# Optimization experiments

Measured on AMD Instinct MI355X. Metric: run time of the kernel, lower is better.

The kernel has to match this reference:

```python
import jax, jax.numpy as jnp
import numpy as np

B, S, E, H = 2, 2048, 1024, 16
D = E // H  # head dim = 64


def setup_inputs() -> dict:
    key = jax.random.key(0)
    k1, k2, k3 = jax.random.split(key, 3)
    x = jax.random.normal(k1, (B, S, E), dtype=jnp.float32)
    W_attn = jax.random.normal(k2, (E, 3 * E), dtype=jnp.float32) * (1.0 / np.sqrt(E))
    b_attn = jnp.zeros((3 * E,), dtype=jnp.float32)
    W_proj = jax.random.normal(k3, (E, E), dtype=jnp.float32) * (1.0 / np.sqrt(E))
    b_proj = jnp.zeros((E,), dtype=jnp.float32)
    return {"x": x, "W_attn": W_attn, "b_attn": b_attn, "W_proj": W_proj, "b_proj": b_proj}


def reference(x, W_attn, b_attn, W_proj, b_proj):
    b, s, e = x.shape
    qkv = x @ W_attn + b_attn                      # (B, S, 3E)
    q, k, v = jnp.split(qkv, 3, axis=-1)
    # (B, S, E) -> (B, H, S, D)
    def heads(t):
        return t.reshape(b, s, H, D).transpose(0, 2, 1, 3)
    q, k, v = heads(q), heads(k), heads(v)
    scale = 1.0 / np.sqrt(D)
    # ring QK^T over world_size=1 == full QK^T; scores (B, H, S, S)
    attn = jnp.einsum("bhqd,bhkd->bhqk", q, k) * scale
    causal = jnp.tril(jnp.ones((s, s), dtype=bool))
    attn = jnp.where(causal[None, None], attn, -jnp.inf)
    attn = jax.nn.softmax(attn, axis=-1)
    # ring AV over world_size=1 == full AV
    y = jnp.einsum("bhqk,bhkd->bhqd", attn, v)     # (B, H, S, D)
    y = y.transpose(0, 2, 1, 3).reshape(b, s, e)   # (B, S, E)
    return y @ W_proj + b_proj
```

## Files before the change

### kernel.cpp

```cpp
#include <hip/hip_runtime.h>
#include <hip/hip_bf16.h>

#define B_ 2
#define S_ 2048
#define E_ 1024
#define H_ 16
#define D_ 64

typedef __attribute__((ext_vector_type(8))) _Float16 half8;
typedef __attribute__((ext_vector_type(4))) _Float16 half4;
typedef __attribute__((ext_vector_type(4))) float floatx4;

__device__ inline void gload16(const _Float16* g, _Float16* l) {
    __builtin_amdgcn_global_load_lds(
        (const __attribute__((address_space(1))) void*)g,
        (__attribute__((address_space(3))) void*)l, 16, 0, 0);
}

__global__ __launch_bounds__(256) void k_prep(const float* __restrict__ x, _Float16* __restrict__ xh,
                                              const float* __restrict__ Wa, _Float16* __restrict__ Wat,
                                              const float* __restrict__ Wp, _Float16* __restrict__ Wpt) {
    __shared__ _Float16 tile[32][33];
    int bid = blockIdx.x, tid = threadIdx.x;
    if (bid < 2048) {
        int i = (bid * 256 + tid) * 8;
        float4 a = *(const float4*)(x + i);
        float4 b = *(const float4*)(x + i + 4);
        half8 o;
        o[0] = (_Float16)a.x; o[1] = (_Float16)a.y; o[2] = (_Float16)a.z; o[3] = (_Float16)a.w;
        o[4] = (_Float16)b.x; o[5] = (_Float16)b.y; o[6] = (_Float16)b.z; o[7] = (_Float16)b.w;
        *(half8*)(xh + i) = o;
        return;
    }
    const float* in;
    _Float16* out;
    int R, C, bx, by;
    if (bid < 5120) {
        int t = bid - 2048;
        in = Wa; out = Wat; R = E_; C = 3 * E_;
        bx = t % 96; by = t / 96;
    } else {
        int t = bid - 5120;
        in = Wp; out = Wpt; R = E_; C = E_;
        bx = t & 31; by = t >> 5;
    }
    int tx = tid & 31, ty = tid >> 5;
    int c0 = bx * 32, r0 = by * 32;
#pragma unroll
    for (int k = 0; k < 4; k++) {
        int r = ty + k * 8;
        tile[r][tx] = (_Float16)in[(size_t)(r0 + r) * C + c0 + tx];
    }
    __syncthreads();
#pragma unroll
    for (int k = 0; k < 4; k++) {
        int r = ty + k * 8;
        out[(size_t)(c0 + r) * R + r0 + tx] = tile[tx][r];
    }
}

template <int MODE>
__global__ __launch_bounds__(256) void k_gemm(const _Float16* __restrict__ A,
                                              const _Float16* __restrict__ Bt,
                                              const float* __restrict__ bias,
                                              void* __restrict__ out0,
                                              _Float16* __restrict__ out1,
                                              _Float16* __restrict__ out2,
                                              int M, int N, int K) {
    __shared__ __align__(16) _Float16 As[128 * 32];
    __shared__ __align__(16) _Float16 Bs[128 * 32];
    int tid = threadIdx.x;
    int lane = tid & 63, w = tid >> 6;
    int wm = w >> 1, wn = w & 1;
    int l15 = lane & 15, quad = lane >> 4;
    int m0 = blockIdx.y * 128, n0 = blockIdx.x * 128;

    floatx4 acc[4][4];
    floatx4 zero = {0.f, 0.f, 0.f, 0.f};
#pragma unroll
    for (int i = 0; i < 4; i++)
#pragma unroll
        for (int j = 0; j < 4; j++) acc[i][j] = zero;

    for (int k0 = 0; k0 < K; k0 += 32) {
        __syncthreads();
#pragma unroll
        for (int c = 0; c < 2; c++) {
            int flat = c * 2048 + tid * 8;
            int row = flat >> 5, col = flat & 31;
            gload16(A + (size_t)(m0 + row) * K + k0 + col, &As[c * 2048 + w * 512]);
            gload16(Bt + (size_t)(n0 + row) * K + k0 + col, &Bs[c * 2048 + w * 512]);
        }
        __syncthreads();
        half8 af[4], bfr[4];
#pragma unroll
        for (int i = 0; i < 4; i++) af[i] = *(const half8*)&As[(wm * 64 + i * 16 + l15) * 32 + quad * 8];
#pragma unroll
        for (int j = 0; j < 4; j++) bfr[j] = *(const half8*)&Bs[(wn * 64 + j * 16 + l15) * 32 + quad * 8];
#pragma unroll
        for (int i = 0; i < 4; i++)
#pragma unroll
            for (int j = 0; j < 4; j++)
                acc[i][j] = __builtin_amdgcn_mfma_f32_16x16x32_f16(af[i], bfr[j], acc[i][j], 0, 0, 0);
    }
#pragma unroll
    for (int j = 0; j < 4; j++) {
        int gcol = n0 + wn * 64 + j * 16 + l15;
        float bj = bias[gcol];
        int sect = gcol >> 10, e = gcol & 1023;
        int hh = e >> 6, dd = e & 63;
#pragma unroll
        for (int i = 0; i < 4; i++) {
            int grow = m0 + wm * 64 + i * 16 + quad * 4;
#pragma unroll
            for (int r = 0; r < 4; r++) {
                float v = acc[i][j][r] + bj;
                if (MODE == 1) {
                    ((float*)out0)[(size_t)(grow + r) * N + gcol] = v;
                } else {
                    int row = grow + r;
                    int bb = row >> 11, ss = row & 2047;
                    size_t hb = (size_t)(bb * H_ + hh);
                    _Float16 v16 = (_Float16)v;
                    if (sect == 0)
                        ((_Float16*)out0)[(hb * S_ + ss) * D_ + dd] = v16;
                    else if (sect == 1)
                        out1[(hb * S_ + ss) * D_ + dd] = v16;
                    else
                        out2[(hb * D_ + dd) * S_ + ss] = v16;
                }
            }
        }
    }
}

__global__ __launch_bounds__(512, 4)
void k_attn(const _Float16* __restrict__ Qh,
            const _Float16* __restrict__ Kh,
            const _Float16* __restrict__ Vt,
            _Float16* __restrict__ y) {
    __shared__ __align__(16) _Float16 smem_h[25600];
    int tid = threadIdx.x;
    int lane = tid & 63, w = tid >> 6;
    int l15 = lane & 15, quad = lane >> 4;
    _Float16* KsB = smem_h;
    _Float16* VsB = smem_h + 8192;
    _Float16* Pw = smem_h + 16384 + w * (16 * 72);

    int bidx = blockIdx.x;
    int bh = 4 * (bidx & 7) + ((bidx >> 3) & 3);
    int qidx = (bidx >> 5) & 7;
    int qb = (bidx >> 8) ? qidx : (15 - qidx);
    int b = bh >> 4, h = bh & 15;

    const size_t hbase = (size_t)bh * (S_ * D_);
    const _Float16* Qp = Qh + hbase;
    const _Float16* Kp = Kh + hbase;
    const _Float16* Vp = Vt + hbase;

    int q0w = qb * 128 + 16 * w;
    int ktd = q0w >> 6;
    int ktmax = 2 * qb + 1;

    int r0 = tid >> 3;
    int cbh = ((tid * 8) & 63) ^ ((r0 & 7) << 3);
    const _Float16* kS = Kp + (size_t)r0 * D_ + cbh;
    const _Float16* vS = Vp + (size_t)r0 * S_ + cbh;

#define STAGE(kt_, buf_)                                             \
    do {                                                             \
        gload16(kS + (size_t)(kt_) * 4096, KsB + (buf_) * 4096 + w * 512); \
        gload16(vS + (size_t)(kt_) * 64, VsB + (buf_) * 4096 + w * 512);   \
    } while (0)

    half8 aq[2];
#pragma unroll
    for (int kk = 0; kk < 2; kk++) {
        half8 q = *(const half8*)(Qp + (size_t)(q0w + l15) * D_ + kk * 32 + quad * 8);
#pragma unroll
        for (int u = 0; u < 8; u++) q[u] *= (_Float16)0.125f;
        aq[kk] = q;
    }

    floatx4 zero = {0.f, 0.f, 0.f, 0.f};
    floatx4 o[4];
#pragma unroll
    for (int f = 0; f < 4; f++) o[f] = zero;
    float l_run = 0.f;

    STAGE(0, 0);
    int cur = 0;
    int swz = (l15 & 7) << 3;
    for (int kt = 0; kt <= ktmax; kt++) {
        __syncthreads();
        if (kt < ktmax) STAGE(kt + 1, cur ^ 1);
        if (kt <= ktd) {
            const _Float16* KC = KsB + cur * 4096;
            const _Float16* VC = VsB + cur * 4096;
            floatx4 sa[4];
#pragma unroll
            for (int jj = 0; jj < 4; jj++) {
                int row = jj * 16 + l15;
                half8 k0 = *(const half8*)&KC[row * 64 + ((quad * 8) ^ swz)];
                half8 k1 = *(const half8*)&KC[row * 64 + ((32 + quad * 8) ^ swz)];
                floatx4 a = zero;
                a = __builtin_amdgcn_mfma_f32_16x16x32_f16(k0, aq[0], a, 0, 0, 0);
                a = __builtin_amdgcn_mfma_f32_16x16x32_f16(k1, aq[1], a, 0, 0, 0);
                sa[jj] = a;
            }
            bool diag = (kt == ktd);
            int k64 = kt * 64;
            float ssum = 0.f;
#pragma unroll
            for (int jj = 0; jj < 4; jj++) {
                half4 pk;
#pragma unroll
                for (int r = 0; r < 4; r++) {
                    float v = __expf(sa[jj][r]);
                    if (diag) {
                        int key = k64 + jj * 16 + quad * 4 + r;
                        int query = q0w + l15;
                        if (key > query) v = 0.f;
                    }
                    ssum += v;
                    pk[r] = (_Float16)v;
                }
                *(half4*)&Pw[l15 * 72 + jj * 16 + quad * 4] = pk;
            }
            ssum += __shfl_xor(ssum, 16);
            ssum += __shfl_xor(ssum, 32);
            l_run += ssum;
#pragma unroll
            for (int kk = 0; kk < 2; kk++) {
                half8 ap = *(const half8*)&Pw[l15 * 72 + kk * 32 + quad * 8];
#pragma unroll
                for (int f = 0; f < 4; f++) {
                    int row = f * 16 + l15;
                    half8 bv = *(const half8*)&VC[row * 64 + ((kk * 32 + quad * 8) ^ swz)];
                    o[f] = __builtin_amdgcn_mfma_f32_16x16x32_f16(ap, bv, o[f], 0, 0, 0);
                }
            }
        }
        cur ^= 1;
    }
#undef STAGE

    float linv[4];
#pragma unroll
    for (int r = 0; r < 4; r++) linv[r] = 1.0f / __shfl(l_run, quad * 4 + r);
#pragma unroll
    for (int f = 0; f < 4; f++)
#pragma unroll
        for (int r = 0; r < 4; r++) {
            int row = q0w + quad * 4 + r;
            y[((size_t)(b * S_ + row)) * E_ + h * D_ + f * 16 + l15] =
                (_Float16)(o[f][r] * linv[r]);
        }
}

extern "C" void kernel_launch(void* const* d_in, const int* in_sizes, int n_in,
                              void* d_out, int out_size, void* d_ws, size_t ws_size,
                              hipStream_t stream) {
    const float* x      = (const float*)d_in[0];
    const float* W_attn = (const float*)d_in[1];
    const float* b_attn = (const float*)d_in[2];
    const float* W_proj = (const float*)d_in[3];
    const float* b_proj = (const float*)d_in[4];
    float* out = (float*)d_out;

    const int M = B_ * S_;
    char* ws = (char*)d_ws;
    _Float16* xh  = (_Float16*)ws; ws += (size_t)M * E_ * 2;
    _Float16* Wat = (_Float16*)ws; ws += (size_t)3 * E_ * E_ * 2;
    _Float16* Wpt = (_Float16*)ws; ws += (size_t)E_ * E_ * 2;
    _Float16* Qh  = (_Float16*)ws; ws += (size_t)M * E_ * 2;
    _Float16* Kh  = (_Float16*)ws; ws += (size_t)M * E_ * 2;
    _Float16* Vt  = (_Float16*)ws; ws += (size_t)M * E_ * 2;
    _Float16* yh  = xh;

    k_prep<<<6144, 256, 0, stream>>>(x, xh, W_attn, Wat, W_proj, Wpt);
    k_gemm<0><<<dim3(3 * E_ / 128, M / 128), 256, 0, stream>>>(xh, Wat, b_attn, Qh, Kh, Vt, M, 3 * E_, E_);
    k_attn<<<512, 512, 0, stream>>>(Qh, Kh, Vt, yh);
    k_gemm<1><<<dim3(E_ / 128, M / 128), 256, 0, stream>>>(yh, Wpt, b_proj, (void*)out, nullptr, nullptr, M, E_, E_);
}
```

Measured before the change: 193.8 us.

## Double-buffer GEMM LDS tiles, swizzle LDS columns, and remap blocks per XCD

```diff
diff --git a/kernel.cpp b/kernel.cpp
--- a/kernel.cpp
+++ b/kernel.cpp
@@ -67,13 +67,17 @@
                                               _Float16* __restrict__ out1,
                                               _Float16* __restrict__ out2,
                                               int M, int N, int K) {
-    __shared__ __align__(16) _Float16 As[128 * 32];
-    __shared__ __align__(16) _Float16 Bs[128 * 32];
+    __shared__ __align__(16) _Float16 AsB[2 * 4096];
+    __shared__ __align__(16) _Float16 BsB[2 * 4096];
     int tid = threadIdx.x;
     int lane = tid & 63, w = tid >> 6;
     int wm = w >> 1, wn = w & 1;
     int l15 = lane & 15, quad = lane >> 4;
-    int m0 = blockIdx.y * 128, n0 = blockIdx.x * 128;
+    int nbx = N >> 7;
+    int xcd = blockIdx.x & 7, s = blockIdx.x >> 3;
+    int by = xcd * 4 + s / nbx;
+    int bx = s % nbx;
+    int m0 = by * 128, n0 = bx * 128;
 
     floatx4 acc[4][4];
     floatx4 zero = {0.f, 0.f, 0.f, 0.f};
@@ -82,27 +86,45 @@
 #pragma unroll
         for (int j = 0; j < 4; j++) acc[i][j] = zero;
 
+    int srow = tid >> 2;
+    int scol = ((tid * 8) & 31) ^ ((srow & 3) << 3);
+    const _Float16* aS0 = A + (size_t)(m0 + srow) * K + scol;
+    const _Float16* aS1 = A + (size_t)(m0 + 64 + srow) * K + scol;
+    const _Float16* bS0 = Bt + (size_t)(n0 + srow) * K + scol;
+    const _Float16* bS1 = Bt + (size_t)(n0 + 64 + srow) * K + scol;
+
+#define GSTAGE(ko_, buf_)                                          \
+    do {                                                           \
+        gload16(aS0 + (ko_), AsB + (buf_) * 4096 + w * 512);       \
+        gload16(aS1 + (ko_), AsB + (buf_) * 4096 + 2048 + w * 512);\
+        gload16(bS0 + (ko_), BsB + (buf_) * 4096 + w * 512);       \
+        gload16(bS1 + (ko_), BsB + (buf_) * 4096 + 2048 + w * 512);\
+    } while (0)
+
+    GSTAGE(0, 0);
+    int cur = 0;
+    int sx = (l15 & 3) << 3;
     for (int k0 = 0; k0 < K; k0 += 32) {
         __syncthreads();
-#pragma unroll
-        for (int c = 0; c < 2; c++) {
-            int flat = c * 2048 + tid * 8;
-            int row = flat >> 5, col = flat & 31;
-            gload16(A + (size_t)(m0 + row) * K + k0 + col, &As[c * 2048 + w * 512]);
-            gload16(Bt + (size_t)(n0 + row) * K + k0 + col, &Bs[c * 2048 + w * 512]);
-        }
-        __syncthreads();
+        if (k0 + 32 < K) GSTAGE(k0 + 32, cur ^ 1);
+        const _Float16* AC = AsB + cur * 4096;
+        const _Float16* BC = BsB + cur * 4096;
         half8 af[4], bfr[4];
 #pragma unroll
-        for (int i = 0; i < 4; i++) af[i] = *(const half8*)&As[(wm * 64 + i * 16 + l15) * 32 + quad * 8];
-#pragma unroll
-        for (int j = 0; j < 4; j++) bfr[j] = *(const half8*)&Bs[(wn * 64 + j * 16 + l15) * 32 + quad * 8];
+        for (int i = 0; i < 4; i++)
+            af[i] = *(const half8*)&AC[(wm * 64 + i * 16 + l15) * 32 + ((quad * 8) ^ sx)];
+#pragma unroll
+        for (int j = 0; j < 4; j++)
+            bfr[j] = *(const half8*)&BC[(wn * 64 + j * 16 + l15) * 32 + ((quad * 8) ^ sx)];
 #pragma unroll
         for (int i = 0; i < 4; i++)
 #pragma unroll
             for (int j = 0; j < 4; j++)
                 acc[i][j] = __builtin_amdgcn_mfma_f32_16x16x32_f16(af[i], bfr[j], acc[i][j], 0, 0, 0);
-    }
+        cur ^= 1;
+    }
+#undef GSTAGE
+
 #pragma unroll
     for (int j = 0; j < 4; j++) {
         int gcol = n0 + wn * 64 + j * 16 + l15;
@@ -279,7 +301,7 @@
     _Float16* yh  = xh;
 
     k_prep<<<6144, 256, 0, stream>>>(x, xh, W_attn, Wat, W_proj, Wpt);
-    k_gemm<0><<<dim3(3 * E_ / 128, M / 128), 256, 0, stream>>>(xh, Wat, b_attn, Qh, Kh, Vt, M, 3 * E_, E_);
+    k_gemm<0><<<768, 256, 0, stream>>>(xh, Wat, b_attn, Qh, Kh, Vt, M, 3 * E_, E_);
     k_attn<<<512, 512, 0, stream>>>(Qh, Kh, Vt, yh);
-    k_gemm<1><<<dim3(E_ / 128, M / 128), 256, 0, stream>>>(yh, Wpt, b_proj, (void*)out, nullptr, nullptr, M, E_, E_);
-}
+    k_gemm<1><<<256, 256, 0, stream>>>(yh, Wpt, b_proj, (void*)out, nullptr, nullptr, M, E_, E_);
+}
```

Result: faster. 185.8 us (-4.1%).
